# Kernel optimization log

Measured on AMD Instinct MI355X. Metric: run time of the kernel, lower is better.

## Reference

```python
import jax, jax.numpy as jnp
import numpy as np

M = 32000   # query points
N = 32000   # support points
H = 32      # neighbors per query
C = 64      # channels
K = 15      # kernel points (shell_sizes=[1,14])
GROUPS = 8
CH_PER_GRP = C // GROUPS   # 8
COUT = K * CH_PER_GRP      # 120
RADIUS = 2.5
SIGMA = 1.0
INF = 1.0e6


def _leaky_relu(x):
    return jnp.where(x >= 0, x, 0.1 * x)


def setup_inputs() -> dict:
    key = jax.random.key(0)
    ks = jax.random.split(key, 9)
    q_pts = jax.random.normal(ks[0], (M, 3), jnp.float32) * RADIUS
    s_pts = jax.random.normal(ks[1], (N, 3), jnp.float32) * RADIUS
    s_feats = jax.random.normal(ks[2], (N, C), jnp.float32)
    neighb_inds = jax.random.randint(ks[3], (M, H), 0, N)
    # kernel points in a sphere of given radius, first point fixed at center
    kp = jax.random.normal(ks[4], (K, 3), jnp.float32)
    kp = kp / (jnp.linalg.norm(kp, axis=1, keepdims=True) + 1e-9)
    r = RADIUS * jax.random.uniform(ks[5], (K, 1), jnp.float32) ** (1.0 / 3.0)
    kp = kp * r
    kernel_points = kp.at[0].set(0.0)
    # kaiming-uniform-ish conv weights (K, C)
    bound = 1.0 / np.sqrt(C)
    weights = jax.random.uniform(ks[6], (K, C), jnp.float32, -bound, bound)
    # alpha_mlp: Linear(C,C) + LeakyReLU(0.1) + Linear(C,Cout, no bias)
    w1 = jax.random.normal(ks[7], (C, C), jnp.float32) * (1.0 / np.sqrt(C))
    b1 = jnp.zeros((C,), jnp.float32)
    w2 = jax.random.normal(ks[8], (C, COUT), jnp.float32) * (1.0 / np.sqrt(C))
    return {"q_pts": q_pts, "s_pts": s_pts, "s_feats": s_feats,
            "neighb_inds": neighb_inds, "kernel_points": kernel_points,
            "weights": weights, "w1": w1, "b1": b1, "w2": w2}


def reference(q_pts, s_pts, s_feats, neighb_inds, kernel_points, weights, w1, b1, w2):
    # --- gather neighbor features (padded with a zero row) ---
    padded_feats = jnp.concatenate([s_feats, jnp.zeros((1, C), s_feats.dtype)], axis=0)
    neighbor_feats = padded_feats[neighb_inds]                      # (M, H, C)

    # --- attention modulations (M == N branch: pooled_feats = s_feats) ---
    pooled_feats = s_feats                                           # (M, C)
    mod = _leaky_relu(pooled_feats @ w1 + b1) @ w2                   # (M, Cout)
    mod = jax.nn.sigmoid(mod).reshape(M, K, CH_PER_GRP, 1)
    conv_w = weights.reshape(1, K, CH_PER_GRP, GROUPS) * mod         # (M, K, cpg, g)
    conv_w = conv_w.reshape(M, K, C)

    # --- kernel-point influences (no-grad in original) ---
    s_pts_pad = jnp.concatenate([s_pts, jnp.full((1, 3), INF, s_pts.dtype)], axis=0)
    neighbors = s_pts_pad[neighb_inds] - q_pts[:, None, :]           # (M, H, 3)
    diff = neighbors[:, :, None, :] - kernel_points[None, None, :, :]  # (M, H, K, 3)
    sq_d = jnp.sum(diff * diff, axis=-1)                             # (M, H, K)
    nn_sq = jnp.min(sq_d, axis=2)                                    # (M, H)
    nn_idx = jnp.argmin(sq_d, axis=2)                                # (M, H)
    infl = jnp.clip(1.0 - jnp.sqrt(nn_sq) / SIGMA, 0.0)              # linear influence
    infl = jax.lax.stop_gradient(infl)

    # --- gather per-neighbor kernel weights, modulate and aggregate ---
    nw = jnp.take_along_axis(conv_w, nn_idx[:, :, None], axis=1)     # (M, H, C)
    nw = nw * infl[:, :, None]
    return jnp.sum(neighbor_feats * nw, axis=1)                      # (M, C)
```

## Files before the change

kernel.cpp:

```cpp
#include <hip/hip_runtime.h>


#define MQ 32000

typedef unsigned short u16;
typedef unsigned int   u32;
typedef __attribute__((ext_vector_type(8))) short bf16x8;
typedef __attribute__((ext_vector_type(4))) float f32x4;

__device__ __forceinline__ float rlf(float v, int l) {
    return __int_as_float(__builtin_amdgcn_readlane(__float_as_int(v), l));
}
__device__ __forceinline__ int rli(int v, int l) {
    return __builtin_amdgcn_readlane(v, l);
}
__device__ __forceinline__ u16 f2bf(float x) {
    u32 u = __float_as_uint(x);
    return (u16)((u + 0x7FFFu + ((u >> 16) & 1u)) >> 16);
}
__device__ __forceinline__ float bf2f(u16 b) {
    return __uint_as_float(((u32)b) << 16);
}

__global__ void prep_weights(const float* __restrict__ w1,
                             const float* __restrict__ w2,
                             u16* __restrict__ w1p,
                             u16* __restrict__ w2p)
{
    const int tid = threadIdx.x;
    for (int i = tid; i < 64 * 64; i += 256) {
        const int k = i >> 6, j = i & 63;
        const int dst = (((k >> 5) * 4 + ((k >> 3) & 3)) * 4 + (j >> 4)) * 128
                        + (j & 15) * 8 + (k & 7);
        w1p[dst] = f2bf(w1[i]);
    }
    for (int i = tid; i < 64 * 128; i += 256) {
        const int k = i >> 7, j = i & 127;
        const int dst = (((k >> 5) * 4 + ((k >> 3) & 3)) * 8 + (j >> 4)) * 128
                        + (j & 15) * 8 + (k & 7);
        w2p[dst] = (j < 120) ? f2bf(w2[k * 120 + j]) : (u16)0;
    }
}

__global__ __launch_bounds__(256, 2)
void mod_mlp_mfma2(const float* __restrict__ s_feats,
                   const u16*   __restrict__ w1p,
                   const float* __restrict__ b1,
                   const u16*   __restrict__ w2p,
                   u16* __restrict__ modw,
                   u16* __restrict__ fb)
{
    __shared__ u16 hb[4][16 * 64];

    const int tid  = threadIdx.x;
    const int lane = tid & 63;
    const int wid  = tid >> 6;
    const int jj   = lane & 15;
    const int rbg  = lane >> 4;
    const int rb   = rbg * 8;
    const int rowC = rbg * 4;

    const int t  = blockIdx.x * 4 + wid;
    const int m0 = t * 16;

    const float* ar = s_feats + (size_t)(m0 + jj) * 64 + rb;
    float4 v0 = *(const float4*)(ar);
    float4 v1 = *(const float4*)(ar + 4);
    float4 v2 = *(const float4*)(ar + 32);
    float4 v3 = *(const float4*)(ar + 36);
    bf16x8 a0, a1;
    a0[0] = (short)f2bf(v0.x); a0[1] = (short)f2bf(v0.y);
    a0[2] = (short)f2bf(v0.z); a0[3] = (short)f2bf(v0.w);
    a0[4] = (short)f2bf(v1.x); a0[5] = (short)f2bf(v1.y);
    a0[6] = (short)f2bf(v1.z); a0[7] = (short)f2bf(v1.w);
    a1[0] = (short)f2bf(v2.x); a1[1] = (short)f2bf(v2.y);
    a1[2] = (short)f2bf(v2.z); a1[3] = (short)f2bf(v2.w);
    a1[4] = (short)f2bf(v3.x); a1[5] = (short)f2bf(v3.y);
    a1[6] = (short)f2bf(v3.z); a1[7] = (short)f2bf(v3.w);

    *(bf16x8*)(fb + (size_t)(m0 + jj) * 64 + rb)      = a0;
    *(bf16x8*)(fb + (size_t)(m0 + jj) * 64 + 32 + rb) = a1;

    float b1v[4];
    #pragma unroll
    for (int nt = 0; nt < 4; ++nt) b1v[nt] = b1[nt * 16 + jj];

    f32x4 acc[4];
    #pragma unroll
    for (int nt = 0; nt < 4; ++nt) {
        const bf16x8 f0 = *(const bf16x8*)(w1p + ((0 * 4 + rbg) * 4 + nt) * 128 + jj * 8);
        const bf16x8 f1 = *(const bf16x8*)(w1p + ((1 * 4 + rbg) * 4 + nt) * 128 + jj * 8);
        f32x4 z = {0.f, 0.f, 0.f, 0.f};
        z = __builtin_amdgcn_mfma_f32_16x16x32_bf16(a0, f0, z, 0, 0, 0);
        acc[nt] = __builtin_amdgcn_mfma_f32_16x16x32_bf16(a1, f1, z, 0, 0, 0);
    }
    u16* hrow = &hb[wid][0];
    #pragma unroll
    for (int nt = 0; nt < 4; ++nt) {
        #pragma unroll
        for (int r = 0; r < 4; ++r) {
            float h = acc[nt][r] + b1v[nt];
            h = (h >= 0.f) ? h : 0.1f * h;
            hrow[(rowC + r) * 64 + nt * 16 + jj] = f2bf(h);
        }
    }
    const bf16x8 ha0 = *(bf16x8*)(hrow + jj * 64 + rb);
    const bf16x8 ha1 = *(bf16x8*)(hrow + jj * 64 + 32 + rb);

    #pragma unroll
    for (int nt = 0; nt < 8; ++nt) {
        const bf16x8 g0 = *(const bf16x8*)(w2p + ((0 * 4 + rbg) * 8 + nt) * 128 + jj * 8);
        const bf16x8 g1 = *(const bf16x8*)(w2p + ((1 * 4 + rbg) * 8 + nt) * 128 + jj * 8);
        f32x4 z = {0.f, 0.f, 0.f, 0.f};
        z = __builtin_amdgcn_mfma_f32_16x16x32_bf16(ha0, g0, z, 0, 0, 0);
        f32x4 c2 = __builtin_amdgcn_mfma_f32_16x16x32_bf16(ha1, g1, z, 0, 0, 0);
        const int j = nt * 16 + jj;
        if (j < 120) {
            #pragma unroll
            for (int r = 0; r < 4; ++r)
                modw[(size_t)(m0 + rowC + r) * 120 + j] =
                    f2bf(1.f / (1.f + __expf(-c2[r])));
        }
    }
}

__global__ __launch_bounds__(256, 4)
void kp_gather_v4(const float* __restrict__ q_pts,
                  const float* __restrict__ s_pts,
                  const u16*   __restrict__ fb,
                  const int*   __restrict__ neighb_inds,
                  const float* __restrict__ kpts,
                  const float* __restrict__ weights,
                  const u32*   __restrict__ modw32,
                  float* __restrict__ out)
{
    __shared__ float wt_lds[15 * 64];
    const int tid = threadIdx.x;
    if (tid < 240) ((float4*)wt_lds)[tid] = ((const float4*)weights)[tid];
    __syncthreads();

    const int lane = tid & 63;
    const int wid  = tid >> 6;
    const int pair = blockIdx.x * 4 + wid;
    const int m0 = pair * 2;

    const int ind = __builtin_nontemporal_load(&neighb_inds[(size_t)m0 * 32 + lane]);

    const int cdiv = lane & 7;
    const int hl   = lane >> 3;
    bf16x8 fv[2][4];
    #pragma unroll
    for (int qq = 0; qq < 2; ++qq)
        #pragma unroll
        for (int cc = 0; cc < 4; ++cc) {
            const int ih = __shfl(ind, qq * 32 + cc * 8 + hl);
            fv[qq][cc] = *(const bf16x8*)(fb + (size_t)(u32)ih * 64 + cdiv * 8);
        }

    const u32 W0 = (lane < 60) ? __builtin_nontemporal_load(&modw32[(size_t)m0 * 60 + lane]) : 0u;
    const u32 W1 = (lane < 60) ? __builtin_nontemporal_load(&modw32[(size_t)(m0 + 1) * 60 + lane]) : 0u;

    const int q = lane >> 5;
    const int m = m0 + q;
    const float qx = q_pts[m * 3 + 0];
    const float qy = q_pts[m * 3 + 1];
    const float qz = q_pts[m * 3 + 2];
    const float px = s_pts[(size_t)ind * 3 + 0] - qx;
    const float py = s_pts[(size_t)ind * 3 + 1] - qy;
    const float pz = s_pts[(size_t)ind * 3 + 2] - qz;
    float best = 1e30f; int bk = 0;
    #pragma unroll
    for (int k = 0; k < 15; ++k) {
        float ex = px - kpts[k * 3 + 0];
        float ey = py - kpts[k * 3 + 1];
        float ez = pz - kpts[k * 3 + 2];
        float d2 = fmaf(ex, ex, fmaf(ey, ey, ez * ez));
        if (d2 < best) { best = d2; bk = k; }
    }
    const float infl = fmaxf(0.f, 1.f - sqrtf(best));

    float acc[2][8];
    #pragma unroll
    for (int qq = 0; qq < 2; ++qq)
        #pragma unroll
        for (int e = 0; e < 8; ++e) acc[qq][e] = 0.f;

    #pragma unroll
    for (int qq = 0; qq < 2; ++qq) {
        #pragma unroll
        for (int cc = 0; cc < 4; ++cc) {
            const int idx = qq * 32 + cc * 8 + hl;
            const int kh  = __shfl(bk, idx);
            const float fl = __shfl(infl, idx);
            const int j = kh * 8 + cdiv;
            const u32 w32 = (u32)__shfl((int)(qq ? W1 : W0), j >> 1);
            const u16 hbf = (j & 1) ? (u16)(w32 >> 16) : (u16)(w32 & 0xffffu);
            const float w = bf2f(hbf) * fl;
            const float4 wa = *(const float4*)&wt_lds[kh * 64 + cdiv * 8];
            const float4 wb = *(const float4*)&wt_lds[kh * 64 + cdiv * 8 + 4];
            const bf16x8 f8 = fv[qq][cc];
            acc[qq][0] = fmaf(bf2f((u16)f8[0]), wa.x * w, acc[qq][0]);
            acc[qq][1] = fmaf(bf2f((u16)f8[1]), wa.y * w, acc[qq][1]);
            acc[qq][2] = fmaf(bf2f((u16)f8[2]), wa.z * w, acc[qq][2]);
            acc[qq][3] = fmaf(bf2f((u16)f8[3]), wa.w * w, acc[qq][3]);
            acc[qq][4] = fmaf(bf2f((u16)f8[4]), wb.x * w, acc[qq][4]);
            acc[qq][5] = fmaf(bf2f((u16)f8[5]), wb.y * w, acc[qq][5]);
            acc[qq][6] = fmaf(bf2f((u16)f8[6]), wb.z * w, acc[qq][6]);
            acc[qq][7] = fmaf(bf2f((u16)f8[7]), wb.w * w, acc[qq][7]);
        }
    }

    #pragma unroll
    for (int step = 8; step <= 32; step <<= 1)
        #pragma unroll
        for (int qq = 0; qq < 2; ++qq)
            #pragma unroll
            for (int e = 0; e < 8; ++e)
                acc[qq][e] += __shfl_xor(acc[qq][e], step);

    if (hl == 0) {
        #pragma unroll
        for (int qq = 0; qq < 2; ++qq) {
            f32x4 o0 = {acc[qq][0], acc[qq][1], acc[qq][2], acc[qq][3]};
            f32x4 o1 = {acc[qq][4], acc[qq][5], acc[qq][6], acc[qq][7]};
            float* dst = out + (size_t)(m0 + qq) * 64 + cdiv * 8;
            __builtin_nontemporal_store(o0, (f32x4*)dst);
            __builtin_nontemporal_store(o1, (f32x4*)(dst + 4));
        }
    }
}

__global__ __launch_bounds__(256, 3)
void mod_mlp(const float* __restrict__ s_feats,
             const float* __restrict__ w1,
             const float* __restrict__ b1,
             const float* __restrict__ w2,
             float* __restrict__ modw)
{
    __shared__ float w1_lds[64 * 64];
    __shared__ float w2_lds[64 * 120 + 8];

    const int tid = threadIdx.x;
    {
        const float4* s1 = (const float4*)w1;
        float4* d1 = (float4*)w1_lds;
        #pragma unroll
        for (int i = 0; i < 4; ++i) d1[tid + 256 * i] = s1[tid + 256 * i];
        const float4* s2 = (const float4*)w2;
        float4* d2 = (float4*)w2_lds;
        for (int i = tid; i < (64 * 120) / 4; i += 256) d2[i] = s2[i];
        if (tid < 8) w2_lds[64 * 120 + tid] = 0.f;
    }
    __syncthreads();

    const int lane = tid & 63;
    const int wid  = tid >> 6;
    const int c    = lane;
    const int nwaves = gridDim.x * 4;
    const int gwave  = blockIdx.x * 4 + wid;
    const float b1v = b1[c];
    const int cB = 64 + ((c < 56) ? c : 55);

    for (int pair = gwave; pair * 2 < MQ; pair += nwaves) {
        const int m0 = pair * 2;
        float f0 = s_feats[(size_t)m0 * 64 + c];
        float f1 = s_feats[(size_t)(m0 + 1) * 64 + c];
        float h0a = b1v, h0b = 0.f, h1a = b1v, h1b = 0.f;
        #pragma unroll
        for (int i = 0; i < 64; i += 2) {
            float wa = w1_lds[i * 64 + c];
            float wb = w1_lds[(i + 1) * 64 + c];
            h0a = fmaf(rlf(f0, i), wa, h0a);
            h0b = fmaf(rlf(f0, i + 1), wb, h0b);
            h1a = fmaf(rlf(f1, i), wa, h1a);
            h1b = fmaf(rlf(f1, i + 1), wb, h1b);
        }
        float h0 = h0a + h0b, h1 = h1a + h1b;
        h0 = (h0 >= 0.f) ? h0 : 0.1f * h0;
        h1 = (h1 >= 0.f) ? h1 : 0.1f * h1;
        float a00 = 0.f, a01 = 0.f, a10 = 0.f, a11 = 0.f;
        #pragma unroll
        for (int i = 0; i < 64; ++i) {
            float wA = w2_lds[i * 120 + c];
            float wB = w2_lds[i * 120 + cB];
            float s0 = rlf(h0, i);
            float s1 = rlf(h1, i);
            a00 = fmaf(s0, wA, a00);
            a01 = fmaf(s0, wB, a01);
            a10 = fmaf(s1, wA, a10);
            a11 = fmaf(s1, wB, a11);
        }
        modw[(size_t)m0 * 120 + c]       = 1.f / (1.f + __expf(-a00));
        modw[(size_t)(m0 + 1) * 120 + c] = 1.f / (1.f + __expf(-a10));
        if (c < 56) {
            modw[(size_t)m0 * 120 + 64 + c]       = 1.f / (1.f + __expf(-a01));
            modw[(size_t)(m0 + 1) * 120 + 64 + c] = 1.f / (1.f + __expf(-a11));
        }
    }
}

__global__ __launch_bounds__(256, 4)
void kp_gather(const float* __restrict__ q_pts,
               const float* __restrict__ s_pts,
               const float* __restrict__ s_feats,
               const int*   __restrict__ neighb_inds,
               const float* __restrict__ kpts,
               const float* __restrict__ weights,
               const float* __restrict__ modw,
               float* __restrict__ out)
{
    __shared__ float wt_lds[15 * 64];
    const int tid = threadIdx.x;
    if (tid < 240) ((float4*)wt_lds)[tid] = ((const float4*)weights)[tid];
    __syncthreads();

    const int lane = tid & 63;
    const int wid  = tid >> 6;
    const int c    = lane;
    const int u    = c >> 3;
    const int pair = blockIdx.x * 4 + wid;
    const int m0 = pair * 2;

    const int q = lane >> 5;
    const int m = m0 + q;
    const int ind = neighb_inds[(size_t)m0 * 32 + lane];
    const float qx = q_pts[m * 3 + 0];
    const float qy = q_pts[m * 3 + 1];
    const float qz = q_pts[m * 3 + 2];
    const float px = s_pts[(size_t)ind * 3 + 0] - qx;
    const float py = s_pts[(size_t)ind * 3 + 1] - qy;
    const float pz = s_pts[(size_t)ind * 3 + 2] - qz;
    float best = 1e30f; int bk = 0;
    #pragma unroll
    for (int k = 0; k < 15; ++k) {
        float ex = px - kpts[k * 3 + 0];
        float ey = py - kpts[k * 3 + 1];
        float ez = pz - kpts[k * 3 + 2];
        float d2 = fmaf(ex, ex, fmaf(ey, ey, ez * ez));
        if (d2 < best) { best = d2; bk = k; }
    }
    const float infl = fmaxf(0.f, 1.f - sqrtf(best));
    const int pk = (ind << 4) | bk;

    const size_t mb0 = (size_t)m0 * 120, mb1 = mb0 + 120;
    const float vA0 = modw[mb0 + c];
    const float vB0 = (c < 56) ? modw[mb0 + 64 + c] : 0.f;
    const float vA1 = modw[mb1 + c];
    const float vB1 = (c < 56) ? modw[mb1 + 64 + c] : 0.f;

    float fv0[32], fv1[32];
    #pragma unroll
    for (int h = 0; h < 32; ++h)
        fv0[h] = s_feats[(size_t)(rli(pk, h) >> 4) * 64 + c];
    #pragma unroll
    for (int h = 0; h < 32; ++h)
        fv1[h] = s_feats[(size_t)(rli(pk, 32 + h) >> 4) * 64 + c];

    float p0 = 0.f, p1 = 0.f, p2 = 0.f, p3 = 0.f;
    #pragma unroll
    for (int h = 0; h < 32; h += 4) {
        #pragma unroll
        for (int j = 0; j < 4; ++j) {
            const int s = rli(pk, h + j);
            const int kh = s & 15;
            const float fl = rlf(infl, h + j);
            const float sv = (kh < 8) ? __shfl(vA0, (kh << 3) + u)
                                      : __shfl(vB0, ((kh - 8) << 3) + u);
            const float w = wt_lds[(kh << 6) + c] * sv * fl;
            float& p = (j == 0) ? p0 : (j == 1) ? p1 : (j == 2) ? p2 : p3;
            p = fmaf(fv0[h + j], w, p);
        }
    }
    const float acc0 = (p0 + p1) + (p2 + p3);

    float r0 = 0.f, r1 = 0.f, r2 = 0.f, r3 = 0.f;
    #pragma unroll
    for (int h = 0; h < 32; h += 4) {
        #pragma unroll
        for (int j = 0; j < 4; ++j) {
            const int s = rli(pk, 32 + h + j);
            const int kh = s & 15;
            const float fl = rlf(infl, 32 + h + j);
            const float sv = (kh < 8) ? __shfl(vA1, (kh << 3) + u)
                                      : __shfl(vB1, ((kh - 8) << 3) + u);
            const float w = wt_lds[(kh << 6) + c] * sv * fl;
            float& p = (j == 0) ? r0 : (j == 1) ? r1 : (j == 2) ? r2 : r3;
            p = fmaf(fv1[h + j], w, p);
        }
    }
    const float acc1 = (r0 + r1) + (r2 + r3);

    out[(size_t)m0 * 64 + c]       = acc0;
    out[(size_t)(m0 + 1) * 64 + c] = acc1;
}

extern "C" void kernel_launch(void* const* d_in, const int* in_sizes, int n_in,
                              void* d_out, int out_size, void* d_ws, size_t ws_size,
                              hipStream_t stream) {
    const float* q_pts       = (const float*)d_in[0];
    const float* s_pts       = (const float*)d_in[1];
    const float* s_feats     = (const float*)d_in[2];
    const int*   neighb_inds = (const int*)d_in[3];
    const float* kpts        = (const float*)d_in[4];
    const float* weights     = (const float*)d_in[5];
    const float* w1          = (const float*)d_in[6];
    const float* b1          = (const float*)d_in[7];
    const float* w2          = (const float*)d_in[8];
    float* out = (float*)d_out;

    const size_t offFB   = 0;
    const size_t offMODW = (size_t)MQ * 64 * sizeof(u16);
    const size_t offW1P  = offMODW + (size_t)MQ * 120 * sizeof(u16);
    const size_t offW2P  = offW1P + 4096 * sizeof(u16);
    const size_t needBF  = offW2P + 8192 * sizeof(u16);
    const size_t needF32 = (size_t)MQ * 120 * sizeof(float);

    if (ws_size >= needBF) {
        u16* fb    = (u16*)((char*)d_ws + offFB);
        u16* modwb = (u16*)((char*)d_ws + offMODW);
        u16* w1p   = (u16*)((char*)d_ws + offW1P);
        u16* w2p   = (u16*)((char*)d_ws + offW2P);
        prep_weights<<<1, 256, 0, stream>>>(w1, w2, w1p, w2p);
        mod_mlp_mfma2<<<500, 256, 0, stream>>>(s_feats, w1p, b1, w2p, modwb, fb);
        kp_gather_v4<<<MQ / 8, 256, 0, stream>>>(q_pts, s_pts, fb, neighb_inds,
                                                 kpts, weights, (const u32*)modwb, out);
    } else if (ws_size >= needF32) {
        float* modw = (float*)d_ws;
        mod_mlp<<<768, 256, 0, stream>>>(s_feats, w1, b1, w2, modw);
        kp_gather<<<MQ / 8, 256, 0, stream>>>(q_pts, s_pts, s_feats, neighb_inds,
                                              kpts, weights, modw, out);
    }
}
```

Baseline: 120.2 us.

## Fuse modulation MLP into gather kernel via LDS, merge bf16 conversion with weight prep

The attention-modulation MLP moves into the gather kernel. Wave 0 of each 512-thread block computes the sigmoid modulations for 16 rows with MFMA and writes them to LDS, while the other waves gather neighbor features and pick the nearest kernel point. This removes the global round trip of the bf16 modulation buffer and one kernel launch. The s_feats-to-bf16 conversion and the weight packing are merged into a single pre-kernel. In exchange, wave 0 does serial MLP work while the other waves wait at a block barrier, and the larger blocks may reduce occupancy.

```diff
diff --git a/kernel.cpp b/kernel.cpp
--- a/kernel.cpp
+++ b/kernel.cpp
@@ -22,129 +22,121 @@
     return __uint_as_float(((u32)b) << 16);
 }
 
-__global__ void prep_weights(const float* __restrict__ w1,
-                             const float* __restrict__ w2,
-                             u16* __restrict__ w1p,
-                             u16* __restrict__ w2p)
+__global__ __launch_bounds__(256)
+void fb_build(const float* __restrict__ s_feats,
+              const float* __restrict__ w1,
+              const float* __restrict__ w2,
+              u16* __restrict__ fb,
+              u16* __restrict__ w1p,
+              u16* __restrict__ w2p)
 {
-    const int tid = threadIdx.x;
-    for (int i = tid; i < 64 * 64; i += 256) {
-        const int k = i >> 6, j = i & 63;
-        const int dst = (((k >> 5) * 4 + ((k >> 3) & 3)) * 4 + (j >> 4)) * 128
-                        + (j & 15) * 8 + (k & 7);
-        w1p[dst] = f2bf(w1[i]);
-    }
-    for (int i = tid; i < 64 * 128; i += 256) {
-        const int k = i >> 7, j = i & 127;
-        const int dst = (((k >> 5) * 4 + ((k >> 3) & 3)) * 8 + (j >> 4)) * 128
-                        + (j & 15) * 8 + (k & 7);
-        w2p[dst] = (j < 120) ? f2bf(w2[k * 120 + j]) : (u16)0;
-    }
-}
-
-__global__ __launch_bounds__(256, 2)
-void mod_mlp_mfma2(const float* __restrict__ s_feats,
-                   const u16*   __restrict__ w1p,
-                   const float* __restrict__ b1,
-                   const u16*   __restrict__ w2p,
-                   u16* __restrict__ modw,
-                   u16* __restrict__ fb)
+    const size_t base = ((size_t)blockIdx.x * 256 + threadIdx.x) * 16;
+    if (base < (size_t)MQ * 64) {
+        const float4* src = (const float4*)(s_feats + base);
+        bf16x8 b0, b1;
+        float4 v0 = src[0], v1 = src[1], v2 = src[2], v3 = src[3];
+        b0[0] = (short)f2bf(v0.x); b0[1] = (short)f2bf(v0.y);
+        b0[2] = (short)f2bf(v0.z); b0[3] = (short)f2bf(v0.w);
+        b0[4] = (short)f2bf(v1.x); b0[5] = (short)f2bf(v1.y);
+        b0[6] = (short)f2bf(v1.z); b0[7] = (short)f2bf(v1.w);
+        b1[0] = (short)f2bf(v2.x); b1[1] = (short)f2bf(v2.y);
+        b1[2] = (short)f2bf(v2.z); b1[3] = (short)f2bf(v2.w);
+        b1[4] = (short)f2bf(v3.x); b1[5] = (short)f2bf(v3.y);
+        b1[6] = (short)f2bf(v3.z); b1[7] = (short)f2bf(v3.w);
+        *(bf16x8*)(fb + base)     = b0;
+        *(bf16x8*)(fb + base + 8) = b1;
+    }
+    if (blockIdx.x == 0) {
+        for (int i = threadIdx.x; i < 64 * 64; i += 256) {
+            const int k = i >> 6, j = i & 63;
+            const int dst = (((k >> 5) * 4 + ((k >> 3) & 3)) * 4 + (j >> 4)) * 128
+                            + (j & 15) * 8 + (k & 7);
+            w1p[dst] = f2bf(w1[i]);
+        }
+    }
+    if (blockIdx.x == 1) {
+        for (int i = threadIdx.x; i < 64 * 128; i += 256) {
+            const int k = i >> 7, j = i & 127;
+            const int dst = (((k >> 5) * 4 + ((k >> 3) & 3)) * 8 + (j >> 4)) * 128
+                            + (j & 15) * 8 + (k & 7);
+            w2p[dst] = (j < 120) ? f2bf(w2[k * 120 + j]) : (u16)0;
+        }
+    }
+}
+
+__global__ __launch_bounds__(512, 4)
+void kp_fused(const float* __restrict__ q_pts,
+              const float* __restrict__ s_pts,
+              const u16*   __restrict__ fb,
+              const int*   __restrict__ neighb_inds,
+              const float* __restrict__ kpts,
+              const float* __restrict__ weights,
+              const u16*   __restrict__ w1p,
+              const float* __restrict__ b1,
+              const u16*   __restrict__ w2p,
+              float* __restrict__ out)
 {
-    __shared__ u16 hb[4][16 * 64];
+    __shared__ float wt_lds[15 * 64];
+    __shared__ float mod_lds[16 * 120];
+    __shared__ u16  hb[16 * 64];
 
     const int tid  = threadIdx.x;
     const int lane = tid & 63;
     const int wid  = tid >> 6;
-    const int jj   = lane & 15;
-    const int rbg  = lane >> 4;
-    const int rb   = rbg * 8;
-    const int rowC = rbg * 4;
-
-    const int t  = blockIdx.x * 4 + wid;
-    const int m0 = t * 16;
-
-    const float* ar = s_feats + (size_t)(m0 + jj) * 64 + rb;
-    float4 v0 = *(const float4*)(ar);
-    float4 v1 = *(const float4*)(ar + 4);
-    float4 v2 = *(const float4*)(ar + 32);
-    float4 v3 = *(const float4*)(ar + 36);
-    bf16x8 a0, a1;
-    a0[0] = (short)f2bf(v0.x); a0[1] = (short)f2bf(v0.y);
-    a0[2] = (short)f2bf(v0.z); a0[3] = (short)f2bf(v0.w);
-    a0[4] = (short)f2bf(v1.x); a0[5] = (short)f2bf(v1.y);
-    a0[6] = (short)f2bf(v1.z); a0[7] = (short)f2bf(v1.w);
-    a1[0] = (short)f2bf(v2.x); a1[1] = (short)f2bf(v2.y);
-    a1[2] = (short)f2bf(v2.z); a1[3] = (short)f2bf(v2.w);
-    a1[4] = (short)f2bf(v3.x); a1[5] = (short)f2bf(v3.y);
-    a1[6] = (short)f2bf(v3.z); a1[7] = (short)f2bf(v3.w);
-
-    *(bf16x8*)(fb + (size_t)(m0 + jj) * 64 + rb)      = a0;
-    *(bf16x8*)(fb + (size_t)(m0 + jj) * 64 + 32 + rb) = a1;
-
-    float b1v[4];
-    #pragma unroll
-    for (int nt = 0; nt < 4; ++nt) b1v[nt] = b1[nt * 16 + jj];
-
-    f32x4 acc[4];
-    #pragma unroll
-    for (int nt = 0; nt < 4; ++nt) {
-        const bf16x8 f0 = *(const bf16x8*)(w1p + ((0 * 4 + rbg) * 4 + nt) * 128 + jj * 8);
-        const bf16x8 f1 = *(const bf16x8*)(w1p + ((1 * 4 + rbg) * 4 + nt) * 128 + jj * 8);
-        f32x4 z = {0.f, 0.f, 0.f, 0.f};
-        z = __builtin_amdgcn_mfma_f32_16x16x32_bf16(a0, f0, z, 0, 0, 0);
-        acc[nt] = __builtin_amdgcn_mfma_f32_16x16x32_bf16(a1, f1, z, 0, 0, 0);
-    }
-    u16* hrow = &hb[wid][0];
-    #pragma unroll
-    for (int nt = 0; nt < 4; ++nt) {
-        #pragma unroll
-        for (int r = 0; r < 4; ++r) {
-            float h = acc[nt][r] + b1v[nt];
-            h = (h >= 0.f) ? h : 0.1f * h;
-            hrow[(rowC + r) * 64 + nt * 16 + jj] = f2bf(h);
-        }
-    }
-    const bf16x8 ha0 = *(bf16x8*)(hrow + jj * 64 + rb);
-    const bf16x8 ha1 = *(bf16x8*)(hrow + jj * 64 + 32 + rb);
-
-    #pragma unroll
-    for (int nt = 0; nt < 8; ++nt) {
-        const bf16x8 g0 = *(const bf16x8*)(w2p + ((0 * 4 + rbg) * 8 + nt) * 128 + jj * 8);
-        const bf16x8 g1 = *(const bf16x8*)(w2p + ((1 * 4 + rbg) * 8 + nt) * 128 + jj * 8);
-        f32x4 z = {0.f, 0.f, 0.f, 0.f};
-        z = __builtin_amdgcn_mfma_f32_16x16x32_bf16(ha0, g0, z, 0, 0, 0);
-        f32x4 c2 = __builtin_amdgcn_mfma_f32_16x16x32_bf16(ha1, g1, z, 0, 0, 0);
-        const int j = nt * 16 + jj;
-        if (j < 120) {
+    const int m0   = blockIdx.x * 16;
+
+    if (tid < 240) ((float4*)wt_lds)[tid] = ((const float4*)weights)[tid];
+
+    if (wid == 0) {
+        const int jj = lane & 15, rbg = lane >> 4;
+        const int rb = rbg * 8, rowC = rbg * 4;
+        const u16* arow = fb + (size_t)(m0 + jj) * 64;
+        const bf16x8 a0 = *(const bf16x8*)(arow + rb);
+        const bf16x8 a1 = *(const bf16x8*)(arow + 32 + rb);
+        float b1v[4];
+        #pragma unroll
+        for (int nt = 0; nt < 4; ++nt) b1v[nt] = b1[nt * 16 + jj];
+
+        f32x4 acc[4];
+        #pragma unroll
+        for (int nt = 0; nt < 4; ++nt) {
+            const bf16x8 f0 = *(const bf16x8*)(w1p + ((0 * 4 + rbg) * 4 + nt) * 128 + jj * 8);
+            const bf16x8 f1 = *(const bf16x8*)(w1p + ((1 * 4 + rbg) * 4 + nt) * 128 + jj * 8);
+            f32x4 z = {0.f, 0.f, 0.f, 0.f};
+            z = __builtin_amdgcn_mfma_f32_16x16x32_bf16(a0, f0, z, 0, 0, 0);
+            acc[nt] = __builtin_amdgcn_mfma_f32_16x16x32_bf16(a1, f1, z, 0, 0, 0);
+        }
+        #pragma unroll
+        for (int nt = 0; nt < 4; ++nt) {
             #pragma unroll
-            for (int r = 0; r < 4; ++r)
-                modw[(size_t)(m0 + rowC + r) * 120 + j] =
-                    f2bf(1.f / (1.f + __expf(-c2[r])));
-        }
-    }
-}
-
-__global__ __launch_bounds__(256, 4)
-void kp_gather_v4(const float* __restrict__ q_pts,
-                  const float* __restrict__ s_pts,
-                  const u16*   __restrict__ fb,
-                  const int*   __restrict__ neighb_inds,
-                  const float* __restrict__ kpts,
-                  const float* __restrict__ weights,
-                  const u32*   __restrict__ modw32,
-                  float* __restrict__ out)
-{
-    __shared__ float wt_lds[15 * 64];
-    const int tid = threadIdx.x;
-    if (tid < 240) ((float4*)wt_lds)[tid] = ((const float4*)weights)[tid];
-    __syncthreads();
-
-    const int lane = tid & 63;
-    const int wid  = tid >> 6;
-    const int pair = blockIdx.x * 4 + wid;
-    const int m0 = pair * 2;
-
-    const int ind = __builtin_nontemporal_load(&neighb_inds[(size_t)m0 * 32 + lane]);
+            for (int r = 0; r < 4; ++r) {
+                float h = acc[nt][r] + b1v[nt];
+                h = (h >= 0.f) ? h : 0.1f * h;
+                hb[(rowC + r) * 64 + nt * 16 + jj] = f2bf(h);
+            }
+        }
+        const bf16x8 ha0 = *(bf16x8*)(hb + jj * 64 + rb);
+        const bf16x8 ha1 = *(bf16x8*)(hb + jj * 64 + 32 + rb);
+
+        #pragma unroll
+        for (int nt = 0; nt < 8; ++nt) {
+            const bf16x8 g0 = *(const bf16x8*)(w2p + ((0 * 4 + rbg) * 8 + nt) * 128 + jj * 8);
+            const bf16x8 g1 = *(const bf16x8*)(w2p + ((1 * 4 + rbg) * 8 + nt) * 128 + jj * 8);
+            f32x4 z = {0.f, 0.f, 0.f, 0.f};
+            z = __builtin_amdgcn_mfma_f32_16x16x32_bf16(ha0, g0, z, 0, 0, 0);
+            f32x4 c2 = __builtin_amdgcn_mfma_f32_16x16x32_bf16(ha1, g1, z, 0, 0, 0);
+            const int j = nt * 16 + jj;
+            if (j < 120) {
+                #pragma unroll
+                for (int r = 0; r < 4; ++r)
+                    mod_lds[(rowC + r) * 120 + j] = 1.f / (1.f + __expf(-c2[r]));
+            }
+        }
+    }
+
+    const int pb  = wid;
+    const int m0p = m0 + pb * 2;
+    const int ind = __builtin_nontemporal_load(&neighb_inds[(size_t)m0p * 32 + lane]);
 
     const int cdiv = lane & 7;
     const int hl   = lane >> 3;
@@ -157,11 +149,8 @@
             fv[qq][cc] = *(const bf16x8*)(fb + (size_t)(u32)ih * 64 + cdiv * 8);
         }
 
-    const u32 W0 = (lane < 60) ? __builtin_nontemporal_load(&modw32[(size_t)m0 * 60 + lane]) : 0u;
-    const u32 W1 = (lane < 60) ? __builtin_nontemporal_load(&modw32[(size_t)(m0 + 1) * 60 + lane]) : 0u;
-
     const int q = lane >> 5;
-    const int m = m0 + q;
+    const int m = m0p + q;
     const float qx = q_pts[m * 3 + 0];
     const float qy = q_pts[m * 3 + 1];
     const float qz = q_pts[m * 3 + 2];
@@ -179,6 +168,8 @@
     }
     const float infl = fmaxf(0.f, 1.f - sqrtf(best));
 
+    __syncthreads();
+
     float acc[2][8];
     #pragma unroll
     for (int qq = 0; qq < 2; ++qq)
@@ -187,15 +178,14 @@
 
     #pragma unroll
     for (int qq = 0; qq < 2; ++qq) {
+        const int row = pb * 2 + qq;
         #pragma unroll
         for (int cc = 0; cc < 4; ++cc) {
             const int idx = qq * 32 + cc * 8 + hl;
             const int kh  = __shfl(bk, idx);
             const float fl = __shfl(infl, idx);
-            const int j = kh * 8 + cdiv;
-            const u32 w32 = (u32)__shfl((int)(qq ? W1 : W0), j >> 1);
-            const u16 hbf = (j & 1) ? (u16)(w32 >> 16) : (u16)(w32 & 0xffffu);
-            const float w = bf2f(hbf) * fl;
+            const float sv = mod_lds[row * 120 + kh * 8 + cdiv];
+            const float w  = sv * fl;
             const float4 wa = *(const float4*)&wt_lds[kh * 64 + cdiv * 8];
             const float4 wb = *(const float4*)&wt_lds[kh * 64 + cdiv * 8 + 4];
             const bf16x8 f8 = fv[qq][cc];
@@ -223,7 +213,7 @@
         for (int qq = 0; qq < 2; ++qq) {
             f32x4 o0 = {acc[qq][0], acc[qq][1], acc[qq][2], acc[qq][3]};
             f32x4 o1 = {acc[qq][4], acc[qq][5], acc[qq][6], acc[qq][7]};
-            float* dst = out + (size_t)(m0 + qq) * 64 + cdiv * 8;
+            float* dst = out + (size_t)(m0p + qq) * 64 + cdiv * 8;
             __builtin_nontemporal_store(o0, (f32x4*)dst);
             __builtin_nontemporal_store(o1, (f32x4*)(dst + 4));
         }
@@ -408,22 +398,19 @@
     const float* w2          = (const float*)d_in[8];
     float* out = (float*)d_out;
 
-    const size_t offFB   = 0;
-    const size_t offMODW = (size_t)MQ * 64 * sizeof(u16);
-    const size_t offW1P  = offMODW + (size_t)MQ * 120 * sizeof(u16);
-    const size_t offW2P  = offW1P + 4096 * sizeof(u16);
-    const size_t needBF  = offW2P + 8192 * sizeof(u16);
+    const size_t offFB  = 0;
+    const size_t offW1P = (size_t)MQ * 64 * sizeof(u16);
+    const size_t offW2P = offW1P + 4096 * sizeof(u16);
+    const size_t needBF = offW2P + 8192 * sizeof(u16);
     const size_t needF32 = (size_t)MQ * 120 * sizeof(float);
 
     if (ws_size >= needBF) {
-        u16* fb    = (u16*)((char*)d_ws + offFB);
-        u16* modwb = (u16*)((char*)d_ws + offMODW);
-        u16* w1p   = (u16*)((char*)d_ws + offW1P);
-        u16* w2p   = (u16*)((char*)d_ws + offW2P);
-        prep_weights<<<1, 256, 0, stream>>>(w1, w2, w1p, w2p);
-        mod_mlp_mfma2<<<500, 256, 0, stream>>>(s_feats, w1p, b1, w2p, modwb, fb);
-        kp_gather_v4<<<MQ / 8, 256, 0, stream>>>(q_pts, s_pts, fb, neighb_inds,
-                                                 kpts, weights, (const u32*)modwb, out);
+        u16* fb  = (u16*)((char*)d_ws + offFB);
+        u16* w1p = (u16*)((char*)d_ws + offW1P);
+        u16* w2p = (u16*)((char*)d_ws + offW2P);
+        fb_build<<<512, 256, 0, stream>>>(s_feats, w1, w2, fb, w1p, w2p);
+        kp_fused<<<MQ / 16, 512, 0, stream>>>(q_pts, s_pts, fb, neighb_inds,
+                                              kpts, weights, w1p, b1, w2p, out);
     } else if (ws_size >= needF32) {
         float* modw = (float*)d_ws;
         mod_mlp<<<768, 256, 0, stream>>>(s_feats, w1, b1, w2, modw);
```

Measured after the change: 119.8 us. No clear change (-0.4%).
